# Kernel tuning notes

Hardware: AMD Instinct MI355X
Metric: run time of the kernel (lower is better)

The kernel has to match this reference:

```python
import jax, jax.numpy as jnp
import numpy as np

U, V, E = 50000, 50000, 800000
F_DIM, G_DIM, H_DIM = 64, 64, 16
G_DIMS = [128, 64]
F_DIMS = [128, 64]


def _glorot(key, fan_in, fan_out):
    lim = np.sqrt(1.0 / fan_in)
    return jax.random.uniform(key, (fan_in, fan_out), jnp.float32, -lim, lim)


def setup_inputs() -> dict:
    key = jax.random.key(0)
    ks = jax.random.split(key, 16)
    inp = {
        "u": jax.random.normal(ks[0], (U, F_DIM), jnp.float32),
        "v": jax.random.normal(ks[1], (V, G_DIM), jnp.float32),
        "e_vals": jax.random.normal(ks[2], (E, H_DIM), jnp.float32),
        "e_idx_v": jax.random.randint(ks[3], (E,), 0, V),
        "e_idx_u": jax.random.randint(ks[4], (E,), 0, U),
        # g MLP: (F+G+H) -> 128 -> 64, ReLU after every layer (output_relu=True)
        "g_w1": _glorot(ks[5], F_DIM + G_DIM + H_DIM, G_DIMS[0]),
        "g_b1": jnp.zeros((G_DIMS[0],), jnp.float32),
        "g_w2": _glorot(ks[6], G_DIMS[0], G_DIMS[1]),
        "g_b2": jnp.zeros((G_DIMS[1],), jnp.float32),
        # f MLP: (F + g_dims[-1]) -> 128 -> 64
        "f_w1": _glorot(ks[7], F_DIM + G_DIMS[1], F_DIMS[0]),
        "f_b1": jnp.zeros((F_DIMS[0],), jnp.float32),
        "f_w2": _glorot(ks[8], F_DIMS[0], F_DIMS[1]),
        "f_b2": jnp.zeros((F_DIMS[1],), jnp.float32),
    }
    return inp


def reference(u, v, e_vals, e_idx_v, e_idx_u, g_w1, g_b1, g_w2, g_b2,
              f_w1, f_b1, f_w2, f_b2):
    # gather endpoint features per edge and concat with edge features: (E, F+G+H)
    x = jnp.concatenate([u[e_idx_u], v[e_idx_v], e_vals], axis=-1)
    # per-edge MLP g with ReLU on every layer
    h = jax.nn.relu(x @ g_w1 + g_b1)
    h = jax.nn.relu(h @ g_w2 + g_b2)  # (E, D)
    # scatter-sum over V side: sum edges sharing the same u index -> (U, D)
    agg = jax.ops.segment_sum(h, e_idx_u, num_segments=u.shape[0])
    # node MLP f on concat[u, aggregated messages]
    y = jax.nn.relu(jnp.concatenate([u, agg], axis=-1) @ f_w1 + f_b1)
    out = jax.nn.relu(y @ f_w2 + f_b2)  # (U, F_DIMS[-1])
    return out
```

## Files before the change

kernel.cpp:

```cpp
#include <hip/hip_runtime.h>

constexpr int U_N = 50000;
constexpr int V_N = 50000;
constexpr int E_N = 800000;

typedef float f32x4 __attribute__((ext_vector_type(4)));
typedef short bf16x8 __attribute__((ext_vector_type(8)));
typedef unsigned short u16x8 __attribute__((ext_vector_type(8)));

__device__ __forceinline__ float relu(float x) { return fmaxf(x, 0.f); }

__device__ __forceinline__ unsigned short f2bf(float f) {
    unsigned u = __float_as_uint(f);
    unsigned rounding = 0x7FFFu + ((u >> 16) & 1u);
    return (unsigned short)((u + rounding) >> 16);
}
__device__ __forceinline__ float bf2f(unsigned short b) {
    return __uint_as_float(((unsigned)b) << 16);
}

constexpr int NB_HIST = (E_N + 255) / 256;
constexpr int NB_PROJ = (U_N + 63) / 64;
constexpr int NBINS = U_N;
constexpr int NSCAN = (NBINS + 1023) / 1024;


__device__ __forceinline__ void proj_mfma(const float* __restrict__ X,
                                          const float* __restrict__ W,
                                          unsigned short* __restrict__ P,
                                          int N, int row0,
                                          unsigned short* sWf)
{
    const int tid = threadIdx.x;

    for (int idx = tid; idx < 64 * 128 / 4; idx += 256) {
        int k  = (idx * 4) >> 7;
        int n0 = (idx * 4) & 127;
        float4 w = *(const float4*)&W[k * 128 + n0];
        int ks = k >> 5, hi = (k & 31) >> 3, j = k & 7;
        float wv[4] = {w.x, w.y, w.z, w.w};
#pragma unroll
        for (int q = 0; q < 4; ++q) {
            int n = n0 + q, nt = n >> 4, lo = n & 15;
            sWf[((ks * 8 + nt) * 64 + hi * 16 + lo) * 8 + j] = f2bf(wv[q]);
        }
    }
    __syncthreads();

    const int wid = tid >> 6, lane = tid & 63;
    const int lo = lane & 15, hi = lane >> 4;
    const int row = row0 + wid * 16 + lo;
    const int rl = (row < N) ? row : (N - 1);

    bf16x8 a0, a1;
    {
        union { bf16x8 v; unsigned short s[8]; } ra, rb;
        float4 x0 = *(const float4*)&X[(size_t)rl * 64 + hi * 8];
        float4 x1 = *(const float4*)&X[(size_t)rl * 64 + hi * 8 + 4];
        ra.s[0] = f2bf(x0.x); ra.s[1] = f2bf(x0.y); ra.s[2] = f2bf(x0.z); ra.s[3] = f2bf(x0.w);
        ra.s[4] = f2bf(x1.x); ra.s[5] = f2bf(x1.y); ra.s[6] = f2bf(x1.z); ra.s[7] = f2bf(x1.w);
        float4 y0 = *(const float4*)&X[(size_t)rl * 64 + 32 + hi * 8];
        float4 y1 = *(const float4*)&X[(size_t)rl * 64 + 32 + hi * 8 + 4];
        rb.s[0] = f2bf(y0.x); rb.s[1] = f2bf(y0.y); rb.s[2] = f2bf(y0.z); rb.s[3] = f2bf(y0.w);
        rb.s[4] = f2bf(y1.x); rb.s[5] = f2bf(y1.y); rb.s[6] = f2bf(y1.z); rb.s[7] = f2bf(y1.w);
        a0 = ra.v; a1 = rb.v;
    }

    const int rbase = row0 + wid * 16 + hi * 4;
    const int ph = lo >> 2, pj = lo & 3;
#pragma unroll
    for (int nt = 0; nt < 8; ++nt) {
        f32x4 acc;
#pragma unroll
        for (int r = 0; r < 4; ++r) acc[r] = 0.f;
        bf16x8 b0 = *(const bf16x8*)&sWf[((0 * 8 + nt) * 64 + lane) * 8];
        bf16x8 b1 = *(const bf16x8*)&sWf[((1 * 8 + nt) * 64 + lane) * 8];
        acc = __builtin_amdgcn_mfma_f32_16x16x32_bf16(a0, b0, acc, 0, 0, 0);
        acc = __builtin_amdgcn_mfma_f32_16x16x32_bf16(a1, b1, acc, 0, 0, 0);
#pragma unroll
        for (int r = 0; r < 4; ++r) {
            int gr = rbase + r;
            if (gr < N) P[(size_t)gr * 128 + ph * 32 + nt * 4 + pj] = f2bf(acc[r]);
        }
    }
}

__global__ __launch_bounds__(256) void prep_kernel(
    const int* __restrict__ idx_u, int* __restrict__ counts,
    const float* __restrict__ u, const float* __restrict__ v,
    const float* __restrict__ gw1, const float* __restrict__ gw2,
    const float* __restrict__ fw1, const float* __restrict__ fw2,
    unsigned short* __restrict__ Up, unsigned short* __restrict__ Vp,
    unsigned short* __restrict__ W2f, unsigned short* __restrict__ Wef,
    unsigned short* __restrict__ F1f, unsigned short* __restrict__ F2f)
{
    __shared__ unsigned short sWf[8192];
    int b = blockIdx.x;

    if (b < NB_PROJ) {
        proj_mfma(u, gw1, Up, U_N, b * 64, sWf);
        return;
    }
    b -= NB_PROJ;
    if (b < NB_PROJ) {
        proj_mfma(v, gw1 + 64 * 128, Vp, V_N, b * 64, sWf);
        return;
    }
    b -= NB_PROJ;
    if (b == 0) {
        const int tid = threadIdx.x;
        for (int t = tid; t < 4 * 4 * 64 * 8; t += 256) {
            int j    = t & 7;
            int lane = (t >> 3) & 63;
            int nt   = (t >> 9) & 3;
            int ks   = t >> 11;
            int n = nt * 16 + (lane & 15);
            int k = ks * 32 + (lane >> 4) * 8 + j;
            W2f[t] = f2bf(gw2[k * 64 + n]);
            F2f[t] = f2bf(fw2[k * 64 + n]);
        }
        const float* gw1e = gw1 + 128 * 128;
        for (int t = tid; t < 8 * 64 * 8; t += 256) {
            int j    = t & 7;
            int lane = (t >> 3) & 63;
            int ct   = t >> 9;
            int c = ct * 16 + (lane & 15);
            int k = (lane >> 4) * 8 + j;
            Wef[t] = (k < 16) ? f2bf(gw1e[k * 128 + c]) : (unsigned short)0;
        }
        for (int t = tid; t < 4 * 8 * 64 * 8; t += 256) {
            int j    = t & 7;
            int lane = (t >> 3) & 63;
            int nt   = (t >> 9) & 7;
            int ks   = t >> 12;
            int n = nt * 16 + (lane & 15);
            int k = ks * 32 + (lane >> 4) * 8 + j;
            F1f[t] = f2bf(fw1[k * 128 + n]);
        }
        return;
    }
    b -= 1;
    int e = b * 256 + threadIdx.x;
    if (e < E_N) atomicAdd(&counts[idx_u[e]], 1);
}

__global__ __launch_bounds__(256) void scan_sums(const int* __restrict__ counts,
                                                 int* __restrict__ bsum)
{
    __shared__ int sred[256];
    const int tid = threadIdx.x;
    int base = blockIdx.x * 1024 + tid * 4;
    int s = 0;
    if (base + 3 < NBINS) {
        int4 c = *(const int4*)&counts[base];
        s = c.x + c.y + c.z + c.w;
    } else {
#pragma unroll
        for (int k = 0; k < 4; ++k) { int i = base + k; if (i < NBINS) s += counts[i]; }
    }
    sred[tid] = s;
    __syncthreads();
    for (int off = 128; off > 0; off >>= 1) {
        if (tid < off) sred[tid] += sred[tid + off];
        __syncthreads();
    }
    if (tid == 0) bsum[blockIdx.x] = sred[0];
}

__global__ __launch_bounds__(512) void scan_bsum(int* __restrict__ bsum)
{
    __shared__ int sScan[512];
    const int tid = threadIdx.x;
    int vIn = (tid < NSCAN) ? bsum[tid] : 0;
    sScan[tid] = vIn;
    __syncthreads();
    for (int off = 1; off < 512; off <<= 1) {
        int val = (tid >= off) ? sScan[tid - off] : 0;
        __syncthreads();
        sScan[tid] += val;
        __syncthreads();
    }
    if (tid < NSCAN) bsum[tid] = sScan[tid] - vIn;
}

__global__ __launch_bounds__(256) void scan_apply(int* __restrict__ counts,
                                                  const int* __restrict__ bsum)
{
    __shared__ int sScan[256];
    const int tid = threadIdx.x;
    int base = blockIdx.x * 1024 + tid * 4;
    int v0 = 0, v1 = 0, v2 = 0, v3 = 0;
    if (base + 3 < NBINS) {
        int4 c = *(const int4*)&counts[base];
        v0 = c.x; v1 = c.y; v2 = c.z; v3 = c.w;
    } else {
        if (base     < NBINS) v0 = counts[base];
        if (base + 1 < NBINS) v1 = counts[base + 1];
        if (base + 2 < NBINS) v2 = counts[base + 2];
        if (base + 3 < NBINS) v3 = counts[base + 3];
    }
    int tsum = v0 + v1 + v2 + v3;
    sScan[tid] = tsum;
    __syncthreads();
    for (int off = 1; off < 256; off <<= 1) {
        int val = (tid >= off) ? sScan[tid - off] : 0;
        __syncthreads();
        sScan[tid] += val;
        __syncthreads();
    }
    int excl = sScan[tid] - tsum + bsum[blockIdx.x];
    if (base     < NBINS) counts[base]     = excl;
    if (base + 1 < NBINS) counts[base + 1] = excl + v0;
    if (base + 2 < NBINS) counts[base + 2] = excl + v0 + v1;
    if (base + 3 < NBINS) counts[base + 3] = excl + v0 + v1 + v2;
}

__global__ __launch_bounds__(256) void permute_kernel(
    const int* __restrict__ idx_u, const int* __restrict__ idx_v,
    const float* __restrict__ ev, int* __restrict__ cursor,
    unsigned int* __restrict__ iuv_s, unsigned short* __restrict__ evs)
{
    int e = blockIdx.x * 256 + threadIdx.x;
    if (e >= E_N) return;
    int iu = idx_u[e];
    int iv = idx_v[e];
    int pos = atomicAdd(&cursor[iu], 1);
    iuv_s[pos] = (unsigned)iu | ((unsigned)iv << 16);

    const float* src = &ev[(size_t)e * 16];
    unsigned short* dst = &evs[(size_t)pos * 16];
#pragma unroll
    for (int q = 0; q < 2; ++q) {
        float4 a = *(const float4*)&src[q * 8];
        float4 b = *(const float4*)&src[q * 8 + 4];
        union { u16x8 v; unsigned short s[8]; } o;
        o.s[0] = f2bf(a.x); o.s[1] = f2bf(a.y); o.s[2] = f2bf(a.z); o.s[3] = f2bf(a.w);
        o.s[4] = f2bf(b.x); o.s[5] = f2bf(b.y); o.s[6] = f2bf(b.z); o.s[7] = f2bf(b.w);
        *(u16x8*)&dst[q * 8] = o.v;
    }
}

__global__ __launch_bounds__(256, 4) void edge_kernel(
    const unsigned short* __restrict__ Up,
    const unsigned short* __restrict__ Vp,
    const unsigned short* __restrict__ evs,
    const unsigned int* __restrict__ iuv_s,
    const unsigned short* __restrict__ Wef,
    const float* __restrict__ gb1,
    const unsigned short* __restrict__ W2f,
    const float* __restrict__ gb2,
    float* __restrict__ agg)
{
    __shared__ unsigned short sH1[64 * 136];
    __shared__ unsigned short sW2f[8192];
    __shared__ float sB1[128];
    __shared__ float sB2[64];
    __shared__ int sIu[64];

    const int tid = threadIdx.x;
    const int e0 = blockIdx.x * 64;
    const int wid = tid >> 6, lane = tid & 63;
    const int lo = lane & 15, hi = lane >> 4;
    const int g = e0 + wid * 16 + lo;

    const unsigned iuv = iuv_s[g];
    const int iu = (int)(iuv & 0xFFFFu);
    const int iv = (int)(iuv >> 16);
    if (hi == 0) sIu[wid * 16 + lo] = iu;

    u16x8 vpv[4];
#pragma unroll
    for (int ctp = 0; ctp < 4; ++ctp)
        vpv[ctp] = *(const u16x8*)&Vp[(size_t)iv * 128 + hi * 32 + ctp * 8];

#pragma unroll
    for (int i = 0; i < 4; ++i)
        *(u16x8*)&sW2f[tid * 8 + i * 2048] = *(const u16x8*)&W2f[tid * 8 + i * 2048];
    if (tid < 32) *(float4*)&sB1[tid * 4] = *(const float4*)&gb1[tid * 4];
    else if (tid < 48) *(float4*)&sB2[(tid - 32) * 4] = *(const float4*)&gb2[(tid - 32) * 4];

    bf16x8 bfrag;
    if (hi < 2) {
        bfrag = *(const bf16x8*)&evs[(size_t)g * 16 + hi * 8];
    } else {
        bfrag = (bf16x8)(short)0;
    }

    f32x4 acc[8];
#pragma unroll
    for (int ct = 0; ct < 8; ++ct) {
#pragma unroll
        for (int r = 0; r < 4; ++r) acc[ct][r] = 0.f;
        bf16x8 a = *(const bf16x8*)&Wef[(size_t)((ct * 64 + lane) * 8)];
        acc[ct] = __builtin_amdgcn_mfma_f32_16x16x32_bf16(a, bfrag, acc[ct], 0, 0, 0);
    }

    __syncthreads();

    const int e_loc = wid * 16 + lo;
#pragma unroll
    for (int ctp = 0; ctp < 4; ++ctp) {
        u16x8 uv = *(const u16x8*)&Up[(size_t)iu * 128 + hi * 32 + ctp * 8];
        u16x8 vv = vpv[ctp];
#pragma unroll
        for (int half = 0; half < 2; ++half) {
            const int ct = ctp * 2 + half;
            const int c0 = ct * 16 + hi * 4;
            float4 b1 = *(const float4*)&sB1[c0];
            ushort4 h;
            h.x = f2bf(relu(acc[ct][0] + b1.x + bf2f(uv[half * 4 + 0]) + bf2f(vv[half * 4 + 0])));
            h.y = f2bf(relu(acc[ct][1] + b1.y + bf2f(uv[half * 4 + 1]) + bf2f(vv[half * 4 + 1])));
            h.z = f2bf(relu(acc[ct][2] + b1.z + bf2f(uv[half * 4 + 2]) + bf2f(vv[half * 4 + 2])));
            h.w = f2bf(relu(acc[ct][3] + b1.w + bf2f(uv[half * 4 + 3]) + bf2f(vv[half * 4 + 3])));
            *(ushort4*)&sH1[e_loc * 136 + c0] = h;
        }
    }

    f32x4 accm[4];
#pragma unroll
    for (int nt = 0; nt < 4; ++nt)
#pragma unroll
        for (int r = 0; r < 4; ++r) accm[nt][r] = 0.f;

#pragma unroll
    for (int ks = 0; ks < 4; ++ks) {
        bf16x8 a = *(const bf16x8*)&sH1[(wid * 16 + lo) * 136 + ks * 32 + hi * 8];
#pragma unroll
        for (int nt = 0; nt < 4; ++nt) {
            bf16x8 b = *(const bf16x8*)&sW2f[((ks * 4 + nt) * 64 + lane) * 8];
            accm[nt] = __builtin_amdgcn_mfma_f32_16x16x32_bf16(a, b, accm[nt], 0, 0, 0);
        }
    }
    __syncthreads();

    float* sH2 = (float*)sH1;
#pragma unroll
    for (int nt = 0; nt < 4; ++nt) {
        int col = nt * 16 + lo;
        float b2v = sB2[col];
        int erow = wid * 16 + hi * 4;
#pragma unroll
        for (int r = 0; r < 4; ++r)
            sH2[(erow + r) * 68 + col] = relu(accm[nt][r] + b2v);
    }

    {
        const int c = tid & 63;
        const int eq0 = wid * 16;
        int   iu_cur = sIu[eq0];
        float running = 0.f;
#pragma unroll
        for (int k = 0; k < 16; ++k) {
            int e = eq0 + k;
            int iu2 = sIu[e];
            if (iu2 != iu_cur) {
                atomicAdd(&agg[(size_t)iu_cur * 64 + c], running);
                running = 0.f;
                iu_cur = iu2;
            }
            running += sH2[e * 68 + c];
        }
        atomicAdd(&agg[(size_t)iu_cur * 64 + c], running);
    }
}

__global__ __launch_bounds__(256) void node_kernel(
    const float* __restrict__ u, const float* __restrict__ agg,
    const unsigned short* __restrict__ F1f, const float* __restrict__ fb1,
    const unsigned short* __restrict__ F2f, const float* __restrict__ fb2,
    float* __restrict__ out, int N)
{
    __shared__ unsigned short sY[64 * 136];
    const int tid = threadIdx.x;
    const int wid = tid >> 6, lane = tid & 63;
    const int lo = lane & 15, hi = lane >> 4;
    const int row0 = blockIdx.x * 64;
    const int row = row0 + wid * 16 + lo;
    const int rl = (row < N) ? row : (N - 1);

    bf16x8 a0, a1, a2, a3;
    {
        union { bf16x8 v; unsigned short s[8]; } r0_, r1_, r2_, r3_;
        float4 x0 = *(const float4*)&u[(size_t)rl * 64 + hi * 8];
        float4 x1 = *(const float4*)&u[(size_t)rl * 64 + hi * 8 + 4];
        float4 x2 = *(const float4*)&u[(size_t)rl * 64 + 32 + hi * 8];
        float4 x3 = *(const float4*)&u[(size_t)rl * 64 + 32 + hi * 8 + 4];
        float4 g0 = *(const float4*)&agg[(size_t)rl * 64 + hi * 8];
        float4 g1 = *(const float4*)&agg[(size_t)rl * 64 + hi * 8 + 4];
        float4 g2 = *(const float4*)&agg[(size_t)rl * 64 + 32 + hi * 8];
        float4 g3 = *(const float4*)&agg[(size_t)rl * 64 + 32 + hi * 8 + 4];
        r0_.s[0] = f2bf(x0.x); r0_.s[1] = f2bf(x0.y); r0_.s[2] = f2bf(x0.z); r0_.s[3] = f2bf(x0.w);
        r0_.s[4] = f2bf(x1.x); r0_.s[5] = f2bf(x1.y); r0_.s[6] = f2bf(x1.z); r0_.s[7] = f2bf(x1.w);
        r1_.s[0] = f2bf(x2.x); r1_.s[1] = f2bf(x2.y); r1_.s[2] = f2bf(x2.z); r1_.s[3] = f2bf(x2.w);
        r1_.s[4] = f2bf(x3.x); r1_.s[5] = f2bf(x3.y); r1_.s[6] = f2bf(x3.z); r1_.s[7] = f2bf(x3.w);
        r2_.s[0] = f2bf(g0.x); r2_.s[1] = f2bf(g0.y); r2_.s[2] = f2bf(g0.z); r2_.s[3] = f2bf(g0.w);
        r2_.s[4] = f2bf(g1.x); r2_.s[5] = f2bf(g1.y); r2_.s[6] = f2bf(g1.z); r2_.s[7] = f2bf(g1.w);
        r3_.s[0] = f2bf(g2.x); r3_.s[1] = f2bf(g2.y); r3_.s[2] = f2bf(g2.z); r3_.s[3] = f2bf(g2.w);
        r3_.s[4] = f2bf(g3.x); r3_.s[5] = f2bf(g3.y); r3_.s[6] = f2bf(g3.z); r3_.s[7] = f2bf(g3.w);
        a0 = r0_.v; a1 = r1_.v; a2 = r2_.v; a3 = r3_.v;
    }

#pragma unroll
    for (int nt = 0; nt < 8; ++nt) {
        f32x4 acc;
#pragma unroll
        for (int r = 0; r < 4; ++r) acc[r] = 0.f;
        bf16x8 b0 = *(const bf16x8*)&F1f[(size_t)(((0 * 8 + nt) * 64 + lane) * 8)];
        bf16x8 b1 = *(const bf16x8*)&F1f[(size_t)(((1 * 8 + nt) * 64 + lane) * 8)];
        bf16x8 b2 = *(const bf16x8*)&F1f[(size_t)(((2 * 8 + nt) * 64 + lane) * 8)];
        bf16x8 b3 = *(const bf16x8*)&F1f[(size_t)(((3 * 8 + nt) * 64 + lane) * 8)];
        acc = __builtin_amdgcn_mfma_f32_16x16x32_bf16(a0, b0, acc, 0, 0, 0);
        acc = __builtin_amdgcn_mfma_f32_16x16x32_bf16(a1, b1, acc, 0, 0, 0);
        acc = __builtin_amdgcn_mfma_f32_16x16x32_bf16(a2, b2, acc, 0, 0, 0);
        acc = __builtin_amdgcn_mfma_f32_16x16x32_bf16(a3, b3, acc, 0, 0, 0);
        int col = nt * 16 + lo;
        float b1v = fb1[col];
        int rbase = wid * 16 + hi * 4;
#pragma unroll
        for (int r = 0; r < 4; ++r)
            sY[(rbase + r) * 136 + col] = f2bf(relu(acc[r] + b1v));
    }

    bf16x8 ya0 = *(const bf16x8*)&sY[(wid * 16 + lo) * 136 + 0 * 32 + hi * 8];
    bf16x8 ya1 = *(const bf16x8*)&sY[(wid * 16 + lo) * 136 + 1 * 32 + hi * 8];
    bf16x8 ya2 = *(const bf16x8*)&sY[(wid * 16 + lo) * 136 + 2 * 32 + hi * 8];
    bf16x8 ya3 = *(const bf16x8*)&sY[(wid * 16 + lo) * 136 + 3 * 32 + hi * 8];
#pragma unroll
    for (int nt = 0; nt < 4; ++nt) {
        f32x4 acc;
#pragma unroll
        for (int r = 0; r < 4; ++r) acc[r] = 0.f;
        bf16x8 b0 = *(const bf16x8*)&F2f[(size_t)(((0 * 4 + nt) * 64 + lane) * 8)];
        bf16x8 b1 = *(const bf16x8*)&F2f[(size_t)(((1 * 4 + nt) * 64 + lane) * 8)];
        bf16x8 b2 = *(const bf16x8*)&F2f[(size_t)(((2 * 4 + nt) * 64 + lane) * 8)];
        bf16x8 b3 = *(const bf16x8*)&F2f[(size_t)(((3 * 4 + nt) * 64 + lane) * 8)];
        acc = __builtin_amdgcn_mfma_f32_16x16x32_bf16(ya0, b0, acc, 0, 0, 0);
        acc = __builtin_amdgcn_mfma_f32_16x16x32_bf16(ya1, b1, acc, 0, 0, 0);
        acc = __builtin_amdgcn_mfma_f32_16x16x32_bf16(ya2, b2, acc, 0, 0, 0);
        acc = __builtin_amdgcn_mfma_f32_16x16x32_bf16(ya3, b3, acc, 0, 0, 0);
        int col = nt * 16 + lo;
        float b2v = fb2[col];
#pragma unroll
        for (int r = 0; r < 4; ++r) {
            int gr = row0 + wid * 16 + hi * 4 + r;
            if (gr < N) out[(size_t)gr * 64 + col] = relu(acc[r] + b2v);
        }
    }
}

extern "C" void kernel_launch(void* const* d_in, const int* in_sizes, int n_in,
                              void* d_out, int out_size, void* d_ws, size_t ws_size,
                              hipStream_t stream)
{
    const float* u   = (const float*)d_in[0];
    const float* v   = (const float*)d_in[1];
    const float* ev  = (const float*)d_in[2];
    const int*   eiv = (const int*)d_in[3];
    const int*   eiu = (const int*)d_in[4];
    const float* gw1 = (const float*)d_in[5];
    const float* gb1 = (const float*)d_in[6];
    const float* gw2 = (const float*)d_in[7];
    const float* gb2 = (const float*)d_in[8];
    const float* fw1 = (const float*)d_in[9];
    const float* fb1 = (const float*)d_in[10];
    const float* fw2 = (const float*)d_in[11];
    const float* fb2 = (const float*)d_in[12];
    float* out = (float*)d_out;

    unsigned short* Up     = (unsigned short*)d_ws;
    unsigned short* Vp     = Up + (size_t)U_N * 128;
    unsigned short* evs    = Vp + (size_t)V_N * 128;
    float*          agg    = (float*)(evs + (size_t)E_N * 16);
    int*            counts = (int*)(agg + (size_t)U_N * 64);
    unsigned int*   iuv_s  = (unsigned int*)(counts + NBINS);
    unsigned short* W2f    = (unsigned short*)(iuv_s + E_N);
    unsigned short* Wef    = W2f + 8192;
    unsigned short* F1f    = Wef + 4096;
    unsigned short* F2f    = F1f + 16384;
    int*            bsum   = (int*)(F2f + 8192);

    hipMemsetAsync(agg, 0, ((size_t)U_N * 64 + NBINS) * sizeof(float), stream);

    dim3 blk(256);
    prep_kernel<<<dim3(2 * NB_PROJ + 1 + NB_HIST), blk, 0, stream>>>(
        eiu, counts, u, v, gw1, gw2, fw1, fw2, Up, Vp, W2f, Wef, F1f, F2f);
    scan_sums<<<dim3(NSCAN), blk, 0, stream>>>(counts, bsum);
    scan_bsum<<<dim3(1), dim3(512), 0, stream>>>(bsum);
    scan_apply<<<dim3(NSCAN), blk, 0, stream>>>(counts, bsum);
    permute_kernel<<<dim3(NB_HIST), blk, 0, stream>>>(
        eiu, eiv, ev, counts, iuv_s, evs);

    edge_kernel<<<dim3(E_N / 64), blk, 0, stream>>>(
        Up, Vp, evs, iuv_s, Wef, gb1, W2f, gb2, agg);
    node_kernel<<<dim3((U_N + 63) / 64), blk, 0, stream>>>(
        u, agg, F1f, fb1, F2f, fb2, out, U_N);
}
```

Baseline: 200.5 us.

## Pre-pack projection weights once and fold block-sum scan into scan_apply

Adds a small pack_kernel that converts the g/f weight matrices to bf16 MFMA fragment layout once, so each projection block reads prepacked weights from global memory instead of re-converting the 64x128 weight into shared memory. The weight packing is also spread over several blocks instead of one serial block in prep_kernel. The separate scan_bsum launch is removed; each scan_apply block instead reduces the preceding block sums itself. This trades one extra launch (pack) for removing another launch and redundant per-block weight conversion and syncs.

```diff
diff --git a/kernel.cpp b/kernel.cpp
--- a/kernel.cpp
+++ b/kernel.cpp
@@ -25,28 +25,70 @@
 constexpr int NSCAN = (NBINS + 1023) / 1024;
 
 
+__global__ __launch_bounds__(256) void pack_kernel(
+    const float* __restrict__ gw1, const float* __restrict__ gw2,
+    const float* __restrict__ fw1, const float* __restrict__ fw2,
+    unsigned short* __restrict__ Upf, unsigned short* __restrict__ Vpf,
+    unsigned short* __restrict__ Wef, unsigned short* __restrict__ W2f,
+    unsigned short* __restrict__ F1f, unsigned short* __restrict__ F2f)
+{
+    const int tid = threadIdx.x;
+    const int b = blockIdx.x;
+
+    if (b == 0 || b == 1) {
+        const float* W = (b == 0) ? gw1 : (gw1 + 64 * 128);
+        unsigned short* P = (b == 0) ? Upf : Vpf;
+        for (int t = tid; t < 2 * 8 * 64 * 8; t += 256) {
+            int j    = t & 7;
+            int lane = (t >> 3) & 63;
+            int nt   = (t >> 9) & 7;
+            int ks   = t >> 12;
+            int n = nt * 16 + (lane & 15);
+            int k = ks * 32 + (lane >> 4) * 8 + j;
+            P[t] = f2bf(W[k * 128 + n]);
+        }
+    } else if (b == 2) {
+        const float* gw1e = gw1 + 128 * 128;
+        for (int t = tid; t < 8 * 64 * 8; t += 256) {
+            int j    = t & 7;
+            int lane = (t >> 3) & 63;
+            int ct   = t >> 9;
+            int c = ct * 16 + (lane & 15);
+            int k = (lane >> 4) * 8 + j;
+            Wef[t] = (k < 16) ? f2bf(gw1e[k * 128 + c]) : (unsigned short)0;
+        }
+    } else if (b == 3 || b == 4) {
+        const float* W = (b == 3) ? gw2 : fw2;
+        unsigned short* P = (b == 3) ? W2f : F2f;
+        for (int t = tid; t < 4 * 4 * 64 * 8; t += 256) {
+            int j    = t & 7;
+            int lane = (t >> 3) & 63;
+            int nt   = (t >> 9) & 3;
+            int ks   = t >> 11;
+            int n = nt * 16 + (lane & 15);
+            int k = ks * 32 + (lane >> 4) * 8 + j;
+            P[t] = f2bf(W[k * 64 + n]);
+        }
+    } else {
+        int half = b - 5;
+        for (int t = tid + half * 8192; t < (half + 1) * 8192; t += 256) {
+            int j    = t & 7;
+            int lane = (t >> 3) & 63;
+            int nt   = (t >> 9) & 7;
+            int ks   = t >> 12;
+            int n = nt * 16 + (lane & 15);
+            int k = ks * 32 + (lane >> 4) * 8 + j;
+            F1f[t] = f2bf(fw1[k * 128 + n]);
+        }
+    }
+}
+
 __device__ __forceinline__ void proj_mfma(const float* __restrict__ X,
-                                          const float* __restrict__ W,
+                                          const unsigned short* __restrict__ Wpf,
                                           unsigned short* __restrict__ P,
-                                          int N, int row0,
-                                          unsigned short* sWf)
+                                          int N, int row0)
 {
     const int tid = threadIdx.x;
-
-    for (int idx = tid; idx < 64 * 128 / 4; idx += 256) {
-        int k  = (idx * 4) >> 7;
-        int n0 = (idx * 4) & 127;
-        float4 w = *(const float4*)&W[k * 128 + n0];
-        int ks = k >> 5, hi = (k & 31) >> 3, j = k & 7;
-        float wv[4] = {w.x, w.y, w.z, w.w};
-#pragma unroll
-        for (int q = 0; q < 4; ++q) {
-            int n = n0 + q, nt = n >> 4, lo = n & 15;
-            sWf[((ks * 8 + nt) * 64 + hi * 16 + lo) * 8 + j] = f2bf(wv[q]);
-        }
-    }
-    __syncthreads();
-
     const int wid = tid >> 6, lane = tid & 63;
     const int lo = lane & 15, hi = lane >> 4;
     const int row = row0 + wid * 16 + lo;
@@ -73,8 +115,8 @@
         f32x4 acc;
 #pragma unroll
         for (int r = 0; r < 4; ++r) acc[r] = 0.f;
-        bf16x8 b0 = *(const bf16x8*)&sWf[((0 * 8 + nt) * 64 + lane) * 8];
-        bf16x8 b1 = *(const bf16x8*)&sWf[((1 * 8 + nt) * 64 + lane) * 8];
+        bf16x8 b0 = *(const bf16x8*)&Wpf[((0 * 8 + nt) * 64 + lane) * 8];
+        bf16x8 b1 = *(const bf16x8*)&Wpf[((1 * 8 + nt) * 64 + lane) * 8];
         acc = __builtin_amdgcn_mfma_f32_16x16x32_bf16(a0, b0, acc, 0, 0, 0);
         acc = __builtin_amdgcn_mfma_f32_16x16x32_bf16(a1, b1, acc, 0, 0, 0);
 #pragma unroll
@@ -88,58 +130,21 @@
 __global__ __launch_bounds__(256) void prep_kernel(
     const int* __restrict__ idx_u, int* __restrict__ counts,
     const float* __restrict__ u, const float* __restrict__ v,
-    const float* __restrict__ gw1, const float* __restrict__ gw2,
-    const float* __restrict__ fw1, const float* __restrict__ fw2,
-    unsigned short* __restrict__ Up, unsigned short* __restrict__ Vp,
-    unsigned short* __restrict__ W2f, unsigned short* __restrict__ Wef,
-    unsigned short* __restrict__ F1f, unsigned short* __restrict__ F2f)
-{
-    __shared__ unsigned short sWf[8192];
+    const unsigned short* __restrict__ Upf, const unsigned short* __restrict__ Vpf,
+    unsigned short* __restrict__ Up, unsigned short* __restrict__ Vp)
+{
     int b = blockIdx.x;
 
     if (b < NB_PROJ) {
-        proj_mfma(u, gw1, Up, U_N, b * 64, sWf);
+        proj_mfma(u, Upf, Up, U_N, b * 64);
         return;
     }
     b -= NB_PROJ;
     if (b < NB_PROJ) {
-        proj_mfma(v, gw1 + 64 * 128, Vp, V_N, b * 64, sWf);
+        proj_mfma(v, Vpf, Vp, V_N, b * 64);
         return;
     }
     b -= NB_PROJ;
-    if (b == 0) {
-        const int tid = threadIdx.x;
-        for (int t = tid; t < 4 * 4 * 64 * 8; t += 256) {
-            int j    = t & 7;
-            int lane = (t >> 3) & 63;
-            int nt   = (t >> 9) & 3;
-            int ks   = t >> 11;
-            int n = nt * 16 + (lane & 15);
-            int k = ks * 32 + (lane >> 4) * 8 + j;
-            W2f[t] = f2bf(gw2[k * 64 + n]);
-            F2f[t] = f2bf(fw2[k * 64 + n]);
-        }
-        const float* gw1e = gw1 + 128 * 128;
-        for (int t = tid; t < 8 * 64 * 8; t += 256) {
-            int j    = t & 7;
-            int lane = (t >> 3) & 63;
-            int ct   = t >> 9;
-            int c = ct * 16 + (lane & 15);
-            int k = (lane >> 4) * 8 + j;
-            Wef[t] = (k < 16) ? f2bf(gw1e[k * 128 + c]) : (unsigned short)0;
-        }
-        for (int t = tid; t < 4 * 8 * 64 * 8; t += 256) {
-            int j    = t & 7;
-            int lane = (t >> 3) & 63;
-            int nt   = (t >> 9) & 7;
-            int ks   = t >> 12;
-            int n = nt * 16 + (lane & 15);
-            int k = ks * 32 + (lane >> 4) * 8 + j;
-            F1f[t] = f2bf(fw1[k * 128 + n]);
-        }
-        return;
-    }
-    b -= 1;
     int e = b * 256 + threadIdx.x;
     if (e < E_N) atomicAdd(&counts[idx_u[e]], 1);
 }
@@ -167,27 +172,22 @@
     if (tid == 0) bsum[blockIdx.x] = sred[0];
 }
 
-__global__ __launch_bounds__(512) void scan_bsum(int* __restrict__ bsum)
-{
-    __shared__ int sScan[512];
-    const int tid = threadIdx.x;
-    int vIn = (tid < NSCAN) ? bsum[tid] : 0;
-    sScan[tid] = vIn;
-    __syncthreads();
-    for (int off = 1; off < 512; off <<= 1) {
-        int val = (tid >= off) ? sScan[tid - off] : 0;
-        __syncthreads();
-        sScan[tid] += val;
-        __syncthreads();
-    }
-    if (tid < NSCAN) bsum[tid] = sScan[tid] - vIn;
-}
-
 __global__ __launch_bounds__(256) void scan_apply(int* __restrict__ counts,
                                                   const int* __restrict__ bsum)
 {
     __shared__ int sScan[256];
     const int tid = threadIdx.x;
+
+    int bs = (tid < blockIdx.x && tid < NSCAN) ? bsum[tid] : 0;
+    sScan[tid] = bs;
+    __syncthreads();
+    for (int off = 128; off > 0; off >>= 1) {
+        if (tid < off) sScan[tid] += sScan[tid + off];
+        __syncthreads();
+    }
+    const int boff = sScan[0];
+    __syncthreads();
+
     int base = blockIdx.x * 1024 + tid * 4;
     int v0 = 0, v1 = 0, v2 = 0, v3 = 0;
     if (base + 3 < NBINS) {
@@ -208,7 +208,7 @@
         sScan[tid] += val;
         __syncthreads();
     }
-    int excl = sScan[tid] - tsum + bsum[blockIdx.x];
+    int excl = sScan[tid] - tsum + boff;
     if (base     < NBINS) counts[base]     = excl;
     if (base + 1 < NBINS) counts[base + 1] = excl + v0;
     if (base + 2 < NBINS) counts[base + 2] = excl + v0 + v1;
@@ -477,15 +477,18 @@
     unsigned short* Wef    = W2f + 8192;
     unsigned short* F1f    = Wef + 4096;
     unsigned short* F2f    = F1f + 16384;
-    int*            bsum   = (int*)(F2f + 8192);
+    unsigned short* Upf    = F2f + 8192;
+    unsigned short* Vpf    = Upf + 8192;
+    int*            bsum   = (int*)(Vpf + 8192);
 
     hipMemsetAsync(agg, 0, ((size_t)U_N * 64 + NBINS) * sizeof(float), stream);
 
     dim3 blk(256);
-    prep_kernel<<<dim3(2 * NB_PROJ + 1 + NB_HIST), blk, 0, stream>>>(
-        eiu, counts, u, v, gw1, gw2, fw1, fw2, Up, Vp, W2f, Wef, F1f, F2f);
+    pack_kernel<<<dim3(7), blk, 0, stream>>>(
+        gw1, gw2, fw1, fw2, Upf, Vpf, Wef, W2f, F1f, F2f);
+    prep_kernel<<<dim3(2 * NB_PROJ + NB_HIST), blk, 0, stream>>>(
+        eiu, counts, u, v, Upf, Vpf, Up, Vp);
     scan_sums<<<dim3(NSCAN), blk, 0, stream>>>(counts, bsum);
-    scan_bsum<<<dim3(1), dim3(512), 0, stream>>>(bsum);
     scan_apply<<<dim3(NSCAN), blk, 0, stream>>>(counts, bsum);
     permute_kernel<<<dim3(NB_HIST), blk, 0, stream>>>(
         eiu, eiv, ev, counts, iuv_s, evs);
```

After: 208.9 us. +4.2%, slower.
